# Optimization experiments

Measured on AMD Instinct MI355X. Metric: run time of the kernel, lower is better.

Reference implementation:

```python
import jax, jax.numpy as jnp
import numpy as np

N_ENT = 100000


def setup_inputs() -> dict:
    key = jax.random.key(0)
    ks = jax.random.split(key, 10)
    B, D, O, R, E = 50000, 128, 128, 8, 200000
    return {
        "embeddings": jax.random.normal(ks[0], (N_ENT, D), dtype=jnp.float32),
        "head_e": jax.random.normal(ks[1], (B, D), dtype=jnp.float32),
        "tail_e": jax.random.normal(ks[2], (B, D), dtype=jnp.float32),
        "relation_kernel": jax.random.normal(ks[3], (R, D, O), dtype=jnp.float32),
        "self_kernel": jax.random.normal(ks[4], (D, O), dtype=jnp.float32),
        "edge_val": jax.random.uniform(ks[5], (R, E), dtype=jnp.float32),
        "head_idx": jax.random.randint(ks[6], (B,), 0, N_ENT, dtype=jnp.int32),
        "tail_idx": jax.random.randint(ks[7], (B,), 0, N_ENT, dtype=jnp.int32),
        "edge_src": jax.random.randint(ks[8], (R, E), 0, N_ENT, dtype=jnp.int32),
        "edge_dst": jax.random.randint(ks[9], (R, E), 0, N_ENT, dtype=jnp.int32),
    }


def reference(embeddings, head_e, tail_e, relation_kernel, self_kernel,
              edge_val, head_idx, tail_idx, edge_src, edge_dst):
    # Per-relation SpMM: sum_emb[r, row] = sum_{edges e of r with src=row} val[e] * embeddings[dst[e]]
    def spmm(src, dst, val):
        return jax.ops.segment_sum(embeddings[dst] * val[:, None], src,
                                   num_segments=embeddings.shape[0])
    sum_emb = jax.vmap(spmm)(edge_src, edge_dst, edge_val)  # [R, N, D]

    head_update = jnp.take(sum_emb, head_idx, axis=1)  # [R, B, D]
    tail_update = jnp.take(sum_emb, tail_idx, axis=1)  # [R, B, D]

    head_output = head_e @ self_kernel + jnp.einsum('rbd,rdo->bo', head_update, relation_kernel)
    tail_output = tail_e @ self_kernel + jnp.einsum('rbd,rdo->bo', tail_update, relation_kernel)
    return (jax.nn.sigmoid(head_output), jax.nn.sigmoid(tail_output))
```

## Files before the change

### kernel.cpp

```cpp
#include <hip/hip_runtime.h>
#include <hip/hip_bf16.h>
#include <math.h>

#define N_ENT 100000
#define NB    50000
#define NE    200000
#define RR    8
#define NETOT (RR * NE)
#define NSEG  (RR * N_ENT)

typedef float f32x4  __attribute__((ext_vector_type(4)));
typedef short s16x8  __attribute__((ext_vector_type(8)));

__device__ __forceinline__ void split2(float x, short& h, short& l)
{
    unsigned uh = __float_as_uint(x) & 0xffff0000u;
    h = (short)(uh >> 16);
    float r = x - __uint_as_float(uh);
    l = (short)(__float_as_uint(r) >> 16);
}

__global__ __launch_bounds__(256)
void ktconv_k(const float* __restrict__ rel_k, const float* __restrict__ self_k,
              short* __restrict__ Kth, short* __restrict__ Ktl)
{
    const int r = blockIdx.x;
    const float* src = (r < 8) ? rel_k + (size_t)r * 16384 : self_k;
    short* oh = Kth + (size_t)r * 16384;
    short* ol = Ktl + (size_t)r * 16384;
    for (int i = 0; i < 64; ++i) {
        int ix = i * 256 + threadIdx.x;
        int d = ix >> 7, o = ix & 127;
        short h, l;
        split2(src[ix], h, l);
        oh[o * 128 + d] = h;
        ol[o * 128 + d] = l;
    }
}

template<bool FINAL>
__global__ __launch_bounds__(256)
void gemm_mfma_k(const float* __restrict__ X,
                 const short* __restrict__ Kth, const short* __restrict__ Ktl,
                 const float* __restrict__ Abuf, const int* __restrict__ idx,
                 float* __restrict__ out, int nrows)
{
    __shared__ short Bh[128][136];
    __shared__ short Bl[128][136];

    const int t     = threadIdx.x;
    const int wv    = t >> 6;
    const int lane  = t & 63;
    const int col16 = lane & 15;
    const int g     = lane >> 4;
    const int rowbase = blockIdx.x * 128 + wv * 32;

    {
        const s16x8* gh = (const s16x8*)Kth;
        const s16x8* gl = (const s16x8*)Ktl;
#pragma unroll
        for (int i = 0; i < 8; ++i) {
            int f = t + i * 256;
            int o = f >> 4, c = f & 15;
            *(s16x8*)&Bh[o][c * 8] = gh[f];
            *(s16x8*)&Bl[o][c * 8] = gl[f];
        }
    }
    __syncthreads();

    f32x4 acc[2][8];
#pragma unroll
    for (int m = 0; m < 2; ++m)
#pragma unroll
        for (int c = 0; c < 8; ++c) acc[m][c] = (f32x4){0.f, 0.f, 0.f, 0.f};

#pragma unroll
    for (int s = 0; s < 4; ++s) {
        s16x8 ah[2], al[2];
#pragma unroll
        for (int m = 0; m < 2; ++m) {
            int r = rowbase + m * 16 + col16;
            if (r > nrows - 1) r = nrows - 1;
            const float* xp = X + (size_t)r * 128 + s * 32 + g * 8;
            float4 u0 = *(const float4*)xp;
            float4 u1 = *(const float4*)(xp + 4);
            float u[8] = {u0.x, u0.y, u0.z, u0.w, u1.x, u1.y, u1.z, u1.w};
#pragma unroll
            for (int j = 0; j < 8; ++j) {
                short h, l; split2(u[j], h, l);
                ah[m][j] = h; al[m][j] = l;
            }
        }
#pragma unroll
        for (int c = 0; c < 8; ++c) {
            s16x8 bh = *(const s16x8*)&Bh[c * 16 + col16][s * 32 + g * 8];
            s16x8 bl = *(const s16x8*)&Bl[c * 16 + col16][s * 32 + g * 8];
#pragma unroll
            for (int m = 0; m < 2; ++m) {
                acc[m][c] = __builtin_amdgcn_mfma_f32_16x16x32_bf16(ah[m], bh, acc[m][c], 0, 0, 0);
                acc[m][c] = __builtin_amdgcn_mfma_f32_16x16x32_bf16(ah[m], bl, acc[m][c], 0, 0, 0);
                acc[m][c] = __builtin_amdgcn_mfma_f32_16x16x32_bf16(al[m], bh, acc[m][c], 0, 0, 0);
            }
        }
    }

#pragma unroll
    for (int m = 0; m < 2; ++m) {
#pragma unroll
        for (int j = 0; j < 4; ++j) {
            int row = rowbase + m * 16 + g * 4 + j;
            if (row >= nrows) continue;
            if (FINAL) {
                int gi = idx[row];
                const float* Ar = Abuf + (size_t)gi * 128;
                float* op = out + (size_t)row * 128;
#pragma unroll
                for (int c = 0; c < 8; ++c) {
                    int col = c * 16 + col16;
                    float x = acc[m][c][j] + Ar[col];
                    op[col] = 1.f / (1.f + __expf(-x));
                }
            } else {
                float* op = out + (size_t)row * 128;
#pragma unroll
                for (int c = 0; c < 8; ++c)
                    op[c * 16 + col16] = acc[m][c][j];
            }
        }
    }
}

__global__ __launch_bounds__(256)
void count_k(const int* __restrict__ edge_src, unsigned* __restrict__ cnt)
{
    int g = blockIdx.x * 256 + threadIdx.x;
    int r = g / NE;
    int src = edge_src[g];
    atomicAdd(&cnt[r * N_ENT + src], 1u);
}

__global__ __launch_bounds__(256)
void scan1_k(const unsigned* __restrict__ cnt, unsigned* __restrict__ offs,
             unsigned* __restrict__ bsum)
{
    __shared__ unsigned s[256];
    const int t = threadIdx.x;
    const int base = blockIdx.x * 1024;
    unsigned v[4], sum = 0;
#pragma unroll
    for (int i = 0; i < 4; ++i) {
        int ix = base + t * 4 + i;
        v[i] = (ix < NSEG) ? cnt[ix] : 0u;
        sum += v[i];
    }
    s[t] = sum; __syncthreads();
    for (int off = 1; off < 256; off <<= 1) {
        unsigned x = (t >= off) ? s[t - off] : 0u;
        __syncthreads();
        s[t] += x;
        __syncthreads();
    }
    unsigned run = s[t] - sum;
#pragma unroll
    for (int i = 0; i < 4; ++i) {
        int ix = base + t * 4 + i;
        if (ix < NSEG) offs[ix] = run;
        run += v[i];
    }
    if (t == 255) bsum[blockIdx.x] = s[255];
}

__global__ __launch_bounds__(256)
void scan2_k(unsigned* __restrict__ bsum, int nb)
{
    __shared__ unsigned s[256];
    __shared__ unsigned carry;
    const int t = threadIdx.x;
    if (t == 0) carry = 0;
    __syncthreads();
    for (int base = 0; base < nb; base += 256) {
        unsigned v = (base + t < nb) ? bsum[base + t] : 0u;
        s[t] = v; __syncthreads();
        for (int off = 1; off < 256; off <<= 1) {
            unsigned x = (t >= off) ? s[t - off] : 0u;
            __syncthreads();
            s[t] += x;
            __syncthreads();
        }
        unsigned tot = s[255];
        unsigned excl = s[t] - v + carry;
        if (base + t < nb) bsum[base + t] = excl;
        __syncthreads();
        if (t == 0) carry += tot;
        __syncthreads();
    }
}

__global__ __launch_bounds__(256)
void scan3_k(unsigned* __restrict__ offs, const unsigned* __restrict__ bsum)
{
    const int base = blockIdx.x * 1024;
    unsigned add = bsum[blockIdx.x];
#pragma unroll
    for (int i = 0; i < 4; ++i) {
        int ix = base + threadIdx.x * 4 + i;
        if (ix < NSEG) offs[ix] += add;
    }
    if (blockIdx.x == 0 && threadIdx.x == 0) offs[NSEG] = NETOT;
}

__global__ __launch_bounds__(256)
void fill_k(const int* __restrict__ edge_src, const int* __restrict__ edge_dst,
            const float* __restrict__ edge_val,
            const unsigned* __restrict__ offs, unsigned* __restrict__ cursor,
            int2* __restrict__ recs)
{
    int g = blockIdx.x * 256 + threadIdx.x;
    int r = g / NE;
    int src = edge_src[g];
    int seg = r * N_ENT + src;
    unsigned pos = offs[seg] + atomicAdd(&cursor[seg], 1u);
    int2 rec;
    rec.x = edge_dst[g];
    rec.y = __float_as_int(edge_val[g]);
    recs[pos] = rec;
}

template<bool FIRST>
__global__ __launch_bounds__(256)
void agg_k(const unsigned* __restrict__ offs_r, const int2* __restrict__ recs,
           const float* __restrict__ Y, float* __restrict__ A)
{
    int wid  = (blockIdx.x * 256 + threadIdx.x) >> 6;
    int lane = threadIdx.x & 63;
    unsigned s0 = offs_r[wid];
    unsigned s1 = offs_r[wid + 1];
    float2 acc = {0.f, 0.f};
    for (unsigned e = s0; e < s1; ++e) {
        int2 rec = recs[e];
        float v = __int_as_float(rec.y);
        float2 y = *(const float2*)(Y + (size_t)rec.x * 128 + lane * 2);
        acc.x = fmaf(v, y.x, acc.x);
        acc.y = fmaf(v, y.y, acc.y);
    }
    float* ap = A + (size_t)wid * 128 + lane * 2;
    if (FIRST) {
        *(float2*)ap = acc;
    } else {
        float2 a = *(const float2*)ap;
        a.x += acc.x; a.y += acc.y;
        *(float2*)ap = a;
    }
}

extern "C" void kernel_launch(void* const* d_in, const int* in_sizes, int n_in,
                              void* d_out, int out_size, void* d_ws, size_t ws_size,
                              hipStream_t stream)
{
    const float* emb      = (const float*)d_in[0];
    const float* head_e   = (const float*)d_in[1];
    const float* tail_e   = (const float*)d_in[2];
    const float* rel_k    = (const float*)d_in[3];
    const float* self_k   = (const float*)d_in[4];
    const float* edge_val = (const float*)d_in[5];
    const int*   head_idx = (const int*)d_in[6];
    const int*   tail_idx = (const int*)d_in[7];
    const int*   edge_src = (const int*)d_in[8];
    const int*   edge_dst = (const int*)d_in[9];
    float* out = (float*)d_out;

    char* p = (char*)d_ws;
    float*    A      = (float*)p;    p += (size_t)N_ENT * 128 * sizeof(float);
    float*    Y      = (float*)p;    p += (size_t)N_ENT * 128 * sizeof(float);
    int2*     recs   = (int2*)p;     p += (size_t)NETOT * sizeof(int2);
    unsigned* cnt    = (unsigned*)p; p += (size_t)NSEG * sizeof(unsigned);
    unsigned* offs   = (unsigned*)p; p += ((size_t)NSEG + 1) * sizeof(unsigned);
    unsigned* bsum   = (unsigned*)p; p += 1024 * sizeof(unsigned);
    short*    Kth    = (short*)p;    p += (size_t)9 * 16384 * sizeof(short);
    short*    Ktl    = (short*)p;    p += (size_t)9 * 16384 * sizeof(short);

    const int NB1 = (NSEG + 1023) / 1024;

    dim3 blk(256);

    ktconv_k<<<9, blk, 0, stream>>>(rel_k, self_k, Kth, Ktl);
    hipMemsetAsync(cnt, 0, (size_t)NSEG * sizeof(unsigned), stream);
    count_k<<<NETOT / 256, blk, 0, stream>>>(edge_src, cnt);
    scan1_k<<<NB1, blk, 0, stream>>>(cnt, offs, bsum);
    scan2_k<<<1, blk, 0, stream>>>(bsum, NB1);
    scan3_k<<<NB1, blk, 0, stream>>>(offs, bsum);
    hipMemsetAsync(cnt, 0, (size_t)NSEG * sizeof(unsigned), stream);
    fill_k<<<NETOT / 256, blk, 0, stream>>>(edge_src, edge_dst, edge_val,
                                            offs, cnt, recs);

    int gy = (N_ENT + 127) / 128;
    int ga = (N_ENT * 64) / 256;
    for (int r = 0; r < RR; ++r) {
        gemm_mfma_k<false><<<gy, blk, 0, stream>>>(
            emb, Kth + (size_t)r * 16384, Ktl + (size_t)r * 16384,
            nullptr, nullptr, Y, N_ENT);
        if (r == 0)
            agg_k<true><<<ga, blk, 0, stream>>>(offs + (size_t)r * N_ENT, recs, Y, A);
        else
            agg_k<false><<<ga, blk, 0, stream>>>(offs + (size_t)r * N_ENT, recs, Y, A);
    }

    int gb = (NB + 127) / 128;
    gemm_mfma_k<true><<<gb, blk, 0, stream>>>(
        head_e, Kth + (size_t)8 * 16384, Ktl + (size_t)8 * 16384,
        A, head_idx, out, NB);
    gemm_mfma_k<true><<<gb, blk, 0, stream>>>(
        tail_e, Kth + (size_t)8 * 16384, Ktl + (size_t)8 * 16384,
        A, tail_idx, out + (size_t)NB * 128, NB);
}
```

Measured before the change: 716.7 us.

## Aggregate raw embeddings first, then apply a fused multi-relation GEMM

Reorders the computation so the per-relation sparse aggregation gathers raw embeddings into a concatenated [N, nrel*128] buffer. A single GEMM with K = nrel*128 then applies all relation kernels at once and accumulates into A. This drops the eight separate embedding×kernel GEMMs and the read-modify-write of A per relation, replacing them with one larger-K GEMM per group of relations. The group size depends on the available workspace; if the workspace is small it falls back to multiple passes with accumulation. The intermediate buffer needs up to 8×N×128 floats.

After: 700.0 us. 1.02x faster.

```diff
diff --git a/kernel.cpp b/kernel.cpp
--- a/kernel.cpp
+++ b/kernel.cpp
@@ -38,10 +38,11 @@
     }
 }
 
-template<bool FINAL>
-__global__ __launch_bounds__(256)
-void gemm_mfma_k(const float* __restrict__ X,
+template<bool FINAL, bool ACCUM>
+__global__ __launch_bounds__(256)
+void gemm_mfma_k(const float* __restrict__ X, int xstride,
                  const short* __restrict__ Kth, const short* __restrict__ Ktl,
+                 int nkc,
                  const float* __restrict__ Abuf, const int* __restrict__ idx,
                  float* __restrict__ out, int nrows)
 {
@@ -55,51 +56,54 @@
     const int g     = lane >> 4;
     const int rowbase = blockIdx.x * 128 + wv * 32;
 
-    {
-        const s16x8* gh = (const s16x8*)Kth;
-        const s16x8* gl = (const s16x8*)Ktl;
-#pragma unroll
-        for (int i = 0; i < 8; ++i) {
-            int f = t + i * 256;
-            int o = f >> 4, c = f & 15;
-            *(s16x8*)&Bh[o][c * 8] = gh[f];
-            *(s16x8*)&Bl[o][c * 8] = gl[f];
-        }
-    }
-    __syncthreads();
-
     f32x4 acc[2][8];
 #pragma unroll
     for (int m = 0; m < 2; ++m)
 #pragma unroll
         for (int c = 0; c < 8; ++c) acc[m][c] = (f32x4){0.f, 0.f, 0.f, 0.f};
 
-#pragma unroll
-    for (int s = 0; s < 4; ++s) {
-        s16x8 ah[2], al[2];
-#pragma unroll
-        for (int m = 0; m < 2; ++m) {
-            int r = rowbase + m * 16 + col16;
-            if (r > nrows - 1) r = nrows - 1;
-            const float* xp = X + (size_t)r * 128 + s * 32 + g * 8;
-            float4 u0 = *(const float4*)xp;
-            float4 u1 = *(const float4*)(xp + 4);
-            float u[8] = {u0.x, u0.y, u0.z, u0.w, u1.x, u1.y, u1.z, u1.w};
-#pragma unroll
-            for (int j = 0; j < 8; ++j) {
-                short h, l; split2(u[j], h, l);
-                ah[m][j] = h; al[m][j] = l;
+    for (int kc = 0; kc < nkc; ++kc) {
+        __syncthreads();
+        {
+            const s16x8* gh = (const s16x8*)(Kth + (size_t)kc * 16384);
+            const s16x8* gl = (const s16x8*)(Ktl + (size_t)kc * 16384);
+#pragma unroll
+            for (int i = 0; i < 8; ++i) {
+                int f = t + i * 256;
+                int o = f >> 4, c = f & 15;
+                *(s16x8*)&Bh[o][c * 8] = gh[f];
+                *(s16x8*)&Bl[o][c * 8] = gl[f];
             }
         }
-#pragma unroll
-        for (int c = 0; c < 8; ++c) {
-            s16x8 bh = *(const s16x8*)&Bh[c * 16 + col16][s * 32 + g * 8];
-            s16x8 bl = *(const s16x8*)&Bl[c * 16 + col16][s * 32 + g * 8];
+        __syncthreads();
+
+#pragma unroll
+        for (int s = 0; s < 4; ++s) {
+            s16x8 ah[2], al[2];
 #pragma unroll
             for (int m = 0; m < 2; ++m) {
-                acc[m][c] = __builtin_amdgcn_mfma_f32_16x16x32_bf16(ah[m], bh, acc[m][c], 0, 0, 0);
-                acc[m][c] = __builtin_amdgcn_mfma_f32_16x16x32_bf16(ah[m], bl, acc[m][c], 0, 0, 0);
-                acc[m][c] = __builtin_amdgcn_mfma_f32_16x16x32_bf16(al[m], bh, acc[m][c], 0, 0, 0);
+                int r = rowbase + m * 16 + col16;
+                if (r > nrows - 1) r = nrows - 1;
+                const float* xp = X + (size_t)r * xstride + kc * 128 + s * 32 + g * 8;
+                float4 u0 = *(const float4*)xp;
+                float4 u1 = *(const float4*)(xp + 4);
+                float u[8] = {u0.x, u0.y, u0.z, u0.w, u1.x, u1.y, u1.z, u1.w};
+#pragma unroll
+                for (int j = 0; j < 8; ++j) {
+                    short h, l; split2(u[j], h, l);
+                    ah[m][j] = h; al[m][j] = l;
+                }
+            }
+#pragma unroll
+            for (int c = 0; c < 8; ++c) {
+                s16x8 bh = *(const s16x8*)&Bh[c * 16 + col16][s * 32 + g * 8];
+                s16x8 bl = *(const s16x8*)&Bl[c * 16 + col16][s * 32 + g * 8];
+#pragma unroll
+                for (int m = 0; m < 2; ++m) {
+                    acc[m][c] = __builtin_amdgcn_mfma_f32_16x16x32_bf16(ah[m], bh, acc[m][c], 0, 0, 0);
+                    acc[m][c] = __builtin_amdgcn_mfma_f32_16x16x32_bf16(ah[m], bl, acc[m][c], 0, 0, 0);
+                    acc[m][c] = __builtin_amdgcn_mfma_f32_16x16x32_bf16(al[m], bh, acc[m][c], 0, 0, 0);
+                }
             }
         }
     }
@@ -110,18 +114,23 @@
         for (int j = 0; j < 4; ++j) {
             int row = rowbase + m * 16 + g * 4 + j;
             if (row >= nrows) continue;
+            float* op = out + (size_t)row * 128;
             if (FINAL) {
                 int gi = idx[row];
                 const float* Ar = Abuf + (size_t)gi * 128;
-                float* op = out + (size_t)row * 128;
 #pragma unroll
                 for (int c = 0; c < 8; ++c) {
                     int col = c * 16 + col16;
                     float x = acc[m][c][j] + Ar[col];
                     op[col] = 1.f / (1.f + __expf(-x));
                 }
+            } else if (ACCUM) {
+#pragma unroll
+                for (int c = 0; c < 8; ++c) {
+                    int col = c * 16 + col16;
+                    op[col] += acc[m][c][j];
+                }
             } else {
-                float* op = out + (size_t)row * 128;
 #pragma unroll
                 for (int c = 0; c < 8; ++c)
                     op[c * 16 + col16] = acc[m][c][j];
@@ -226,31 +235,25 @@
     recs[pos] = rec;
 }
 
-template<bool FIRST>
-__global__ __launch_bounds__(256)
-void agg_k(const unsigned* __restrict__ offs_r, const int2* __restrict__ recs,
-           const float* __restrict__ Y, float* __restrict__ A)
+__global__ __launch_bounds__(256)
+void segsum_k(const unsigned* __restrict__ offs_r, const int2* __restrict__ recs,
+              const float* __restrict__ emb, float* __restrict__ B, int nrel)
 {
     int wid  = (blockIdx.x * 256 + threadIdx.x) >> 6;
     int lane = threadIdx.x & 63;
-    unsigned s0 = offs_r[wid];
-    unsigned s1 = offs_r[wid + 1];
+    int j = wid / N_ENT;
+    int s = wid - j * N_ENT;
+    unsigned e0 = offs_r[wid];
+    unsigned e1 = offs_r[wid + 1];
     float2 acc = {0.f, 0.f};
-    for (unsigned e = s0; e < s1; ++e) {
+    for (unsigned e = e0; e < e1; ++e) {
         int2 rec = recs[e];
         float v = __int_as_float(rec.y);
-        float2 y = *(const float2*)(Y + (size_t)rec.x * 128 + lane * 2);
+        float2 y = *(const float2*)(emb + (size_t)rec.x * 128 + lane * 2);
         acc.x = fmaf(v, y.x, acc.x);
         acc.y = fmaf(v, y.y, acc.y);
     }
-    float* ap = A + (size_t)wid * 128 + lane * 2;
-    if (FIRST) {
-        *(float2*)ap = acc;
-    } else {
-        float2 a = *(const float2*)ap;
-        a.x += acc.x; a.y += acc.y;
-        *(float2*)ap = a;
-    }
+    *(float2*)(B + ((size_t)s * nrel + j) * 128 + lane * 2) = acc;
 }
 
 extern "C" void kernel_launch(void* const* d_in, const int* in_sizes, int n_in,
@@ -270,17 +273,26 @@
     float* out = (float*)d_out;
 
     char* p = (char*)d_ws;
-    float*    A      = (float*)p;    p += (size_t)N_ENT * 128 * sizeof(float);
-    float*    Y      = (float*)p;    p += (size_t)N_ENT * 128 * sizeof(float);
-    int2*     recs   = (int2*)p;     p += (size_t)NETOT * sizeof(int2);
-    unsigned* cnt    = (unsigned*)p; p += (size_t)NSEG * sizeof(unsigned);
-    unsigned* offs   = (unsigned*)p; p += ((size_t)NSEG + 1) * sizeof(unsigned);
-    unsigned* bsum   = (unsigned*)p; p += 1024 * sizeof(unsigned);
-    short*    Kth    = (short*)p;    p += (size_t)9 * 16384 * sizeof(short);
-    short*    Ktl    = (short*)p;    p += (size_t)9 * 16384 * sizeof(short);
+    auto take = [&](size_t bytes) -> char* {
+        char* q = p; p += (bytes + 255) & ~(size_t)255; return q;
+    };
+    float*    A    = (float*)take((size_t)N_ENT * 128 * sizeof(float));
+    int2*     recs = (int2*)take((size_t)NETOT * sizeof(int2));
+    unsigned* cnt  = (unsigned*)take((size_t)NSEG * sizeof(unsigned));
+    unsigned* offs = (unsigned*)take(((size_t)NSEG + 1) * sizeof(unsigned));
+    unsigned* bsum = (unsigned*)take(1024 * sizeof(unsigned));
+    short*    Kth  = (short*)take((size_t)9 * 16384 * sizeof(short));
+    short*    Ktl  = (short*)take((size_t)9 * 16384 * sizeof(short));
+    float*    Bbuf = (float*)p;
+
+    size_t used    = (size_t)(p - (char*)d_ws);
+    size_t avail   = (ws_size > used) ? ws_size - used : 0;
+    size_t per_rel = (size_t)N_ENT * 128 * sizeof(float);
+    int RPG = (int)(avail / per_rel);
+    if (RPG > RR) RPG = RR;
+    if (RPG < 1)  RPG = 1;
 
     const int NB1 = (NSEG + 1023) / 1024;
-
     dim3 blk(256);
 
     ktconv_k<<<9, blk, 0, stream>>>(rel_k, self_k, Kth, Ktl);
@@ -293,23 +305,32 @@
     fill_k<<<NETOT / 256, blk, 0, stream>>>(edge_src, edge_dst, edge_val,
                                             offs, cnt, recs);
 
-    int gy = (N_ENT + 127) / 128;
-    int ga = (N_ENT * 64) / 256;
-    for (int r = 0; r < RR; ++r) {
-        gemm_mfma_k<false><<<gy, blk, 0, stream>>>(
-            emb, Kth + (size_t)r * 16384, Ktl + (size_t)r * 16384,
-            nullptr, nullptr, Y, N_ENT);
-        if (r == 0)
-            agg_k<true><<<ga, blk, 0, stream>>>(offs + (size_t)r * N_ENT, recs, Y, A);
+    const int gy = (N_ENT + 127) / 128;
+    int first = 1;
+    for (int g0 = 0; g0 < RR; ) {
+        int nr = (RR - g0 < RPG) ? RR - g0 : RPG;
+        int gs = nr * (N_ENT / 4);
+        segsum_k<<<gs, blk, 0, stream>>>(offs + (size_t)g0 * N_ENT, recs,
+                                         emb, Bbuf, nr);
+        if (first)
+            gemm_mfma_k<false, false><<<gy, blk, 0, stream>>>(
+                Bbuf, nr * 128,
+                Kth + (size_t)g0 * 16384, Ktl + (size_t)g0 * 16384, nr,
+                nullptr, nullptr, A, N_ENT);
         else
-            agg_k<false><<<ga, blk, 0, stream>>>(offs + (size_t)r * N_ENT, recs, Y, A);
-    }
-
-    int gb = (NB + 127) / 128;
-    gemm_mfma_k<true><<<gb, blk, 0, stream>>>(
-        head_e, Kth + (size_t)8 * 16384, Ktl + (size_t)8 * 16384,
+            gemm_mfma_k<false, true><<<gy, blk, 0, stream>>>(
+                Bbuf, nr * 128,
+                Kth + (size_t)g0 * 16384, Ktl + (size_t)g0 * 16384, nr,
+                nullptr, nullptr, A, N_ENT);
+        first = 0;
+        g0 += nr;
+    }
+
+    const int gb = (NB + 127) / 128;
+    gemm_mfma_k<true, false><<<gb, blk, 0, stream>>>(
+        head_e, 128, Kth + (size_t)8 * 16384, Ktl + (size_t)8 * 16384, 1,
         A, head_idx, out, NB);
-    gemm_mfma_k<true><<<gb, blk, 0, stream>>>(
-        tail_e, Kth + (size_t)8 * 16384, Ktl + (size_t)8 * 16384,
+    gemm_mfma_k<true, false><<<gb, blk, 0, stream>>>(
+        tail_e, 128, Kth + (size_t)8 * 16384, Ktl + (size_t)8 * 16384, 1,
         A, tail_idx, out + (size_t)NB * 128, NB);
 }
```
